# Optimization experiments

Hardware: AMD Instinct MI355X
Metric: run time of the kernel (lower is better)

The kernel has to match this reference:

```python
import jax, jax.numpy as jnp
import numpy as np

B, V, H = 128, 50257, 2048   # batch, vocab, history length
NEG_INF = jnp.float32(-jnp.inf)
TEMP_MIN = 1e-5


def setup_inputs() -> dict:
    key = jax.random.key(0)
    k1, k2, k3 = jax.random.split(key, 3)
    logits = jax.random.normal(k1, (B, V), jnp.float32) * 4.0
    previous_tokens = jax.random.randint(k2, (B, H), 0, V)
    # uniform noise for the exponential-race (Gumbel-max) draw; strictly positive
    u = jax.random.uniform(k3, (B, V), jnp.float32, minval=1e-10, maxval=1.0)
    return {
        "logits": logits,
        "previous_tokens": previous_tokens,
        "u": u,
        "top_p": jnp.full((1,), 0.9, jnp.float32),
        "repetition_penalty": jnp.full((1,), 1.35, jnp.float32),
        "temperature": jnp.full((1,), 0.7, jnp.float32),
        "top_k": 50,
    }


def _logits_to_probs(logits, previous_tokens, temperature, top_k, top_p, repetition_penalty):
    b = jnp.arange(logits.shape[0])[:, None]  # [B,1] row index for scatters
    # repetition penalty: gather history scores, shrink, scatter back
    score = jnp.take_along_axis(logits, previous_tokens, axis=1)          # [B,H]
    score = jnp.where(score < 0, score * repetition_penalty, score / repetition_penalty)
    logits = logits.at[b, previous_tokens].set(score)                     # [B,V]
    # nucleus (top-p) filtering via descending sort + cumulative softmax
    order = jnp.argsort(-logits, axis=-1)                                 # [B,V]
    sorted_logits = jnp.take_along_axis(logits, order, axis=1)
    cum_probs = jnp.cumsum(jax.nn.softmax(sorted_logits, axis=-1), axis=-1)
    remove_sorted = cum_probs > top_p
    remove_sorted = remove_sorted.at[:, 0].set(False)                     # keep best token
    # scatter removal mask back to vocab order (order is a permutation)
    remove = jnp.zeros_like(remove_sorted).at[b, order].set(remove_sorted)
    logits = jnp.where(remove, NEG_INF, logits)
    # temperature + top-k pivot filter
    logits = logits / jnp.maximum(temperature, TEMP_MIN)
    v = jax.lax.top_k(logits, top_k)[0]                                   # [B,top_k]
    pivot = v[:, -1:]
    logits = jnp.where(logits < pivot, NEG_INF, logits)
    return jax.nn.softmax(logits, axis=-1)


def reference(logits, previous_tokens, u, top_p, repetition_penalty, temperature, top_k):
    previous_tokens = previous_tokens.astype(jnp.int32)
    probs = _logits_to_probs(logits, previous_tokens, temperature, top_k, top_p,
                             repetition_penalty)
    # multinomial_sample_one_no_sync: exponential race argmax(probs / Exp(1))
    q = -jnp.log(u)
    idx_next = jnp.argmax(probs / q, axis=-1, keepdims=True).astype(jnp.int32)
    return idx_next, probs
```

## Files before the change

kernel.cpp:

```cpp
#include <hip/hip_runtime.h>
#include <cfloat>
#include <cmath>
#include <cstdint>

#define VV 50257
#define SPLITS 8
#define CHUNKA 6284
#define BMW ((CHUNKA + 31) / 32)
#define CAPC 256
#define K1T 256
#define NWAVE (K1T / 64)
#define K2T 512
#define CEXP 28.0f

__device__ __forceinline__ unsigned fmono(float f) {
    unsigned b = __float_as_uint(f);
    return b ^ (((int)b < 0) ? 0xFFFFFFFFu : 0x80000000u);
}
__device__ __forceinline__ float unmono(unsigned m) {
    unsigned b = (m & 0x80000000u) ? (m ^ 0x80000000u) : ~m;
    return __uint_as_float(b);
}
__device__ __forceinline__ uint64_t mkkey(unsigned mono, int idx) {
    return ((uint64_t)mono << 32) | (unsigned)(~idx);
}

__global__ __launch_bounds__(K1T) void pp_k1(
    const float* __restrict__ logits, const int* __restrict__ prev,
    const float* __restrict__ rpp,
    float* __restrict__ ps, uint64_t* __restrict__ gkey,
    float* __restrict__ out_probs, int Hp)
{
    const int sp = blockIdx.x, row = blockIdx.y;
    const int tid = threadIdx.x, lane = tid & 63, wid = tid >> 6;
    const int c0 = sp * CHUNKA;
    const int c1 = min(VV, c0 + CHUNKA);
    const int len = c1 - c0;
    const float rp = rpp[0], inv_rp = 1.0f / rp;

    __shared__ unsigned bm[BMW];
    __shared__ float vals[CHUNKA];
    __shared__ uint64_t kls[K1T];
    __shared__ uint64_t cand[CAPC];
    __shared__ uint64_t top64[64];
    __shared__ float red_s[NWAVE];
    __shared__ uint64_t sV64;
    __shared__ int sCnt, sCnt2;

    for (int i = tid; i < BMW; i += K1T) bm[i] = 0u;
    if (tid == 0) sCnt = 0;
    __syncthreads();

    const int* prow = prev + (size_t)row * Hp;
    const int h4 = Hp >> 2;
    const int4* prow4 = (const int4*)prow;
    for (int i = tid; i < h4; i += K1T) {
        int4 t4 = prow4[i];
        int t;
        t = t4.x; if (t >= c0 && t < c1) { int o = t - c0; atomicOr(&bm[o >> 5], 1u << (o & 31)); }
        t = t4.y; if (t >= c0 && t < c1) { int o = t - c0; atomicOr(&bm[o >> 5], 1u << (o & 31)); }
        t = t4.z; if (t >= c0 && t < c1) { int o = t - c0; atomicOr(&bm[o >> 5], 1u << (o & 31)); }
        t = t4.w; if (t >= c0 && t < c1) { int o = t - c0; atomicOr(&bm[o >> 5], 1u << (o & 31)); }
    }
    for (int i = 4 * h4 + tid; i < Hp; i += K1T) {
        int t = prow[i];
        if (t >= c0 && t < c1) { int o = t - c0; atomicOr(&bm[o >> 5], 1u << (o & 31)); }
    }
    __syncthreads();

    const float* lrow = logits + (size_t)row * VV;
    float* orow = out_probs + (size_t)row * VV;
    const int pad = (4 - (row & 3)) & 3;
    const int n4 = (len - pad) >> 2;
    const int tail0 = pad + 4 * n4;
    const float4* l4 = (const float4*)(lrow + c0 + pad);
    float4* o4 = (float4*)(orow + c0 + pad);
    const float4 z4 = make_float4(0.f, 0.f, 0.f, 0.f);

    float s = 0.0f;
    uint64_t k0 = 0ull;
    for (int o = tid; o < pad; o += K1T) {
        float x = lrow[c0 + o];
        if ((bm[o >> 5] >> (o & 31)) & 1u) x = (x < 0.f) ? x * rp : x * inv_rp;
        vals[o] = x;
        s += __expf(x - CEXP);
        uint64_t a = mkkey(fmono(x), c0 + o);
        k0 = (a > k0) ? a : k0;
    }
    #pragma unroll 4
    for (int k = tid; k < n4; k += K1T) {
        float4 v = l4[k];
        const int ob = pad + 4 * k;
        float x;
        x = v.x; if ((bm[(ob+0) >> 5] >> ((ob+0) & 31)) & 1u) x = (x < 0.f) ? x * rp : x * inv_rp;
        vals[ob + 0] = x; s += __expf(x - CEXP);
        { uint64_t a = mkkey(fmono(x), c0 + ob + 0); k0 = (a > k0) ? a : k0; }
        x = v.y; if ((bm[(ob+1) >> 5] >> ((ob+1) & 31)) & 1u) x = (x < 0.f) ? x * rp : x * inv_rp;
        vals[ob + 1] = x; s += __expf(x - CEXP);
        { uint64_t a = mkkey(fmono(x), c0 + ob + 1); k0 = (a > k0) ? a : k0; }
        x = v.z; if ((bm[(ob+2) >> 5] >> ((ob+2) & 31)) & 1u) x = (x < 0.f) ? x * rp : x * inv_rp;
        vals[ob + 2] = x; s += __expf(x - CEXP);
        { uint64_t a = mkkey(fmono(x), c0 + ob + 2); k0 = (a > k0) ? a : k0; }
        x = v.w; if ((bm[(ob+3) >> 5] >> ((ob+3) & 31)) & 1u) x = (x < 0.f) ? x * rp : x * inv_rp;
        vals[ob + 3] = x; s += __expf(x - CEXP);
        { uint64_t a = mkkey(fmono(x), c0 + ob + 3); k0 = (a > k0) ? a : k0; }
    }
    for (int o = tail0 + tid; o < len; o += K1T) {
        float x = lrow[c0 + o];
        if ((bm[o >> 5] >> (o & 31)) & 1u) x = (x < 0.f) ? x * rp : x * inv_rp;
        vals[o] = x;
        s += __expf(x - CEXP);
        uint64_t a = mkkey(fmono(x), c0 + o);
        k0 = (a > k0) ? a : k0;
    }

    #pragma unroll
    for (int off = 32; off; off >>= 1) s += __shfl_down(s, off);
    if (lane == 0) red_s[wid] = s;

    {
        uint64_t v = k0;
        #pragma unroll
        for (int kk = 2; kk <= 64; kk <<= 1) {
            #pragma unroll
            for (int j = kk >> 1; j > 0; j >>= 1) {
                uint64_t o = __shfl_xor(v, j);
                bool lower = (lane & j) == 0;
                bool asc = (lane & kk) == 0;
                uint64_t mx = (v > o) ? v : o;
                uint64_t mn = (v > o) ? o : v;
                v = (lower != asc) ? mx : mn;
            }
        }
        kls[wid * 64 + (63 - lane)] = v;
    }
    __syncthreads();

    const int slot = row * SPLITS + sp;
    if (tid == 0) {
        float S = red_s[0];
        #pragma unroll
        for (int w = 1; w < NWAVE; ++w) S += red_s[w];
        ps[slot] = S;
    }

    {
        const uint64_t ki = kls[tid];
        int r = tid & 63;
        const int j = tid >> 6;
        #pragma unroll
        for (int o = 0; o < NWAVE; ++o) {
            if (o == j) continue;
            const uint64_t* ls = &kls[o * 64];
            int lo = 0, hi = 64;
            while (lo < hi) {
                int mid = (lo + hi) >> 1;
                if (ls[mid] > ki) lo = mid + 1; else hi = mid;
            }
            r += lo;
        }
        if (r == 63) sV64 = ki;
    }
    __syncthreads();
    const uint64_t th = sV64;

    for (int o = tid; o < len; o += K1T) {
        float x = vals[o];
        uint64_t a = mkkey(fmono(x), c0 + o);
        if (a >= th) {
            int p = atomicAdd(&sCnt, 1);
            if (p < CAPC) cand[p] = a;
        }
    }
    __syncthreads();
    int cnt = sCnt;

    for (int o = tid; o < pad; o += K1T) orow[c0 + o] = 0.0f;
    for (int k = tid; k < n4; k += K1T) o4[k] = z4;
    for (int o = tail0 + tid; o < len; o += K1T) orow[c0 + o] = 0.0f;

    if (cnt > CAPC) {
        uint64_t loK = th, hiK = ~0ull;
        uint64_t thF = th;
        for (int it = 0; it < 64; ++it) {
            uint64_t mid = loK + ((hiK - loK) >> 1);
            if (mid == loK) { thF = hiK; break; }
            if (tid == 0) sCnt2 = 0;
            __syncthreads();
            int lc = 0;
            for (int o = tid; o < len; o += K1T) {
                float x = vals[o];
                lc += (int)(mkkey(fmono(x), c0 + o) >= mid);
            }
            #pragma unroll
            for (int off = 32; off; off >>= 1) lc += __shfl_down(lc, off);
            if (lane == 0) atomicAdd(&sCnt2, lc);
            __syncthreads();
            int c = sCnt2;
            __syncthreads();
            if (c >= 64 && c <= CAPC) { thF = mid; break; }
            if (c > CAPC) loK = mid; else hiK = mid;
        }
        if (tid == 0) sCnt = 0;
        __syncthreads();
        for (int o = tid; o < len; o += K1T) {
            float x = vals[o];
            uint64_t a = mkkey(fmono(x), c0 + o);
            if (a >= thF) {
                int p = atomicAdd(&sCnt, 1);
                if (p < CAPC) cand[p] = a;
            }
        }
        __syncthreads();
        cnt = min(sCnt, CAPC);
    }

    for (int t = tid; t < cnt; t += K1T) {
        const uint64_t ki = cand[t];
        int r = 0;
        int j = 0;
        for (; j + 8 <= cnt; j += 8) {
            uint64_t a0 = cand[j],   a1 = cand[j+1], a2 = cand[j+2], a3 = cand[j+3];
            uint64_t a4 = cand[j+4], a5 = cand[j+5], a6 = cand[j+6], a7 = cand[j+7];
            r += (int)(a0 > ki) + (int)(a1 > ki) + (int)(a2 > ki) + (int)(a3 > ki)
               + (int)(a4 > ki) + (int)(a5 > ki) + (int)(a6 > ki) + (int)(a7 > ki);
        }
        for (; j < cnt; ++j) r += (int)(cand[j] > ki);
        if (r < 64) top64[r] = ki;
    }
    __syncthreads();
    if (tid < 64) gkey[(size_t)slot * 64 + tid] = top64[tid];
}

__global__ __launch_bounds__(K2T) void pp_k2(
    const float* __restrict__ u, const float* __restrict__ toppp,
    const float* __restrict__ tempp, const int* __restrict__ topkp,
    const float* __restrict__ ps, const uint64_t* __restrict__ gkey,
    float* __restrict__ out_idx, float* __restrict__ out_probs)
{
    const int row = blockIdx.x, tid = threadIdx.x;
    __shared__ uint64_t ck[SPLITS * 64];
    __shared__ uint64_t tk[64];
    __shared__ float sS;

    ck[tid] = gkey[(size_t)row * (SPLITS * 64) + tid];
    if (tid == 0) {
        float S = 0.0f;
        #pragma unroll
        for (int j = 0; j < SPLITS; ++j) S += ps[row * SPLITS + j];
        sS = S;
    }
    __syncthreads();

    {
        const int j = tid >> 6;
        const uint64_t ki = ck[tid];
        int r = tid & 63;
        #pragma unroll
        for (int o = 0; o < SPLITS; ++o) {
            if (o == j) continue;
            const uint64_t* ls = &ck[o * 64];
            int lo = 0, hi = 64;
            while (lo < hi) {
                int mid = (lo + hi) >> 1;
                if (ls[mid] > ki) lo = mid + 1; else hi = mid;
            }
            r += lo;
        }
        if (r < 64) tk[r] = ki;
    }
    __syncthreads();

    if (tid < 64) {
        const int lane = tid;
        const float top_p = toppp[0];
        const float temp = tempp[0];
        int K = topkp[0]; K = min(max(K, 1), 64);
        const float Ssum = sS;
        const uint64_t k64 = tk[lane];
        const float vl = unmono((unsigned)(k64 >> 32));
        const int ci = (int)(~(unsigned)(k64 & 0xFFFFFFFFu));
        bool act = (lane < K);
        float e = act ? expf(vl - CEXP) / Ssum : 0.0f;
        float cum = e;
        #pragma unroll
        for (int off2 = 1; off2 < 64; off2 <<= 1) {
            float pv = __shfl_up(cum, off2);
            if (lane >= off2) cum += pv;
        }
        unsigned long long bal = __ballot(act && (cum <= top_p));
        int n = (int)__popcll(bal);
        if (n < 1) n = 1;
        const float v0 = __shfl(vl, 0);
        const float invT = 1.0f / fmaxf(temp, 1e-5f);
        bool keep = (lane < n);
        float w = keep ? expf((vl - v0) * invT) : 0.0f;
        float Z = w;
        #pragma unroll
        for (int off2 = 32; off2; off2 >>= 1) Z += __shfl_xor(Z, off2);
        float p = keep ? (w / Z) : 0.0f;
        if (keep) out_probs[(size_t)row * VV + ci] = p;
        float ratio = -1.0f;
        if (keep) ratio = p / (-logf(u[(size_t)row * VV + ci]));
        int bi = keep ? ci : 0x7FFFFFFF;
        #pragma unroll
        for (int off2 = 32; off2; off2 >>= 1) {
            float orat = __shfl_xor(ratio, off2);
            int oidx = __shfl_xor(bi, off2);
            if (orat > ratio || (orat == ratio && oidx < bi)) { ratio = orat; bi = oidx; }
        }
        if (lane == 0) out_idx[row] = (float)bi;
    }
}

extern "C" void kernel_launch(void* const* d_in, const int* in_sizes, int n_in,
                              void* d_out, int out_size, void* d_ws, size_t ws_size,
                              hipStream_t stream) {
    const float* logits = (const float*)d_in[0];
    const int*   prev   = (const int*)d_in[1];
    const float* u      = (const float*)d_in[2];
    const float* topp   = (const float*)d_in[3];
    const float* rp     = (const float*)d_in[4];
    const float* temp   = (const float*)d_in[5];
    const int*   topk   = (const int*)d_in[6];

    const int B  = in_sizes[0] / VV;
    const int Hp = in_sizes[1] / B;

    char* ws = (char*)d_ws;
    float* ps = (float*)ws;
    uint64_t* gkey = (uint64_t*)(ws + 16384);

    float* out = (float*)d_out;
    pp_k1<<<dim3(SPLITS, B), K1T, 0, stream>>>(
        logits, prev, rp, ps, gkey, out + B, Hp);
    pp_k2<<<B, K2T, 0, stream>>>(
        u, topp, temp, topk, ps, gkey, out, out + B);
}
```

Measured before the change: 31.89 us.

## Drop LDS value staging, re-read logits from global, double block size

Removes the 25KB shared-memory array holding penalized chunk values. The candidate pass and fallback search now reload logits from global memory (likely L2-resident) and reapply the penalty. The output-zeroing stores are folded into the first load loop, and threads per block and candidate capacity are doubled to 512. The intent is higher occupancy with less LDS and more parallel threads per chunk, at the cost of a second global read of each chunk and recomputing the penalty.

```diff
diff --git a/kernel.cpp b/kernel.cpp
--- a/kernel.cpp
+++ b/kernel.cpp
@@ -7,8 +7,8 @@
 #define SPLITS 8
 #define CHUNKA 6284
 #define BMW ((CHUNKA + 31) / 32)
-#define CAPC 256
-#define K1T 256
+#define CAPC 512
+#define K1T 512
 #define NWAVE (K1T / 64)
 #define K2T 512
 #define CEXP 28.0f
@@ -39,7 +39,6 @@
     const float rp = rpp[0], inv_rp = 1.0f / rp;
 
     __shared__ unsigned bm[BMW];
-    __shared__ float vals[CHUNKA];
     __shared__ uint64_t kls[K1T];
     __shared__ uint64_t cand[CAPC];
     __shared__ uint64_t top64[64];
@@ -77,12 +76,18 @@
     float4* o4 = (float4*)(orow + c0 + pad);
     const float4 z4 = make_float4(0.f, 0.f, 0.f, 0.f);
 
+    auto keyAt = [&](int o) -> uint64_t {
+        float x = lrow[c0 + o];
+        if ((bm[o >> 5] >> (o & 31)) & 1u) x = (x < 0.f) ? x * rp : x * inv_rp;
+        return mkkey(fmono(x), c0 + o);
+    };
+
     float s = 0.0f;
     uint64_t k0 = 0ull;
     for (int o = tid; o < pad; o += K1T) {
         float x = lrow[c0 + o];
+        orow[c0 + o] = 0.0f;
         if ((bm[o >> 5] >> (o & 31)) & 1u) x = (x < 0.f) ? x * rp : x * inv_rp;
-        vals[o] = x;
         s += __expf(x - CEXP);
         uint64_t a = mkkey(fmono(x), c0 + o);
         k0 = (a > k0) ? a : k0;
@@ -90,25 +95,26 @@
     #pragma unroll 4
     for (int k = tid; k < n4; k += K1T) {
         float4 v = l4[k];
+        o4[k] = z4;
         const int ob = pad + 4 * k;
         float x;
         x = v.x; if ((bm[(ob+0) >> 5] >> ((ob+0) & 31)) & 1u) x = (x < 0.f) ? x * rp : x * inv_rp;
-        vals[ob + 0] = x; s += __expf(x - CEXP);
+        s += __expf(x - CEXP);
         { uint64_t a = mkkey(fmono(x), c0 + ob + 0); k0 = (a > k0) ? a : k0; }
         x = v.y; if ((bm[(ob+1) >> 5] >> ((ob+1) & 31)) & 1u) x = (x < 0.f) ? x * rp : x * inv_rp;
-        vals[ob + 1] = x; s += __expf(x - CEXP);
+        s += __expf(x - CEXP);
         { uint64_t a = mkkey(fmono(x), c0 + ob + 1); k0 = (a > k0) ? a : k0; }
         x = v.z; if ((bm[(ob+2) >> 5] >> ((ob+2) & 31)) & 1u) x = (x < 0.f) ? x * rp : x * inv_rp;
-        vals[ob + 2] = x; s += __expf(x - CEXP);
+        s += __expf(x - CEXP);
         { uint64_t a = mkkey(fmono(x), c0 + ob + 2); k0 = (a > k0) ? a : k0; }
         x = v.w; if ((bm[(ob+3) >> 5] >> ((ob+3) & 31)) & 1u) x = (x < 0.f) ? x * rp : x * inv_rp;
-        vals[ob + 3] = x; s += __expf(x - CEXP);
+        s += __expf(x - CEXP);
         { uint64_t a = mkkey(fmono(x), c0 + ob + 3); k0 = (a > k0) ? a : k0; }
     }
     for (int o = tail0 + tid; o < len; o += K1T) {
         float x = lrow[c0 + o];
+        orow[c0 + o] = 0.0f;
         if ((bm[o >> 5] >> (o & 31)) & 1u) x = (x < 0.f) ? x * rp : x * inv_rp;
-        vals[o] = x;
         s += __expf(x - CEXP);
         uint64_t a = mkkey(fmono(x), c0 + o);
         k0 = (a > k0) ? a : k0;
@@ -164,34 +170,40 @@
     __syncthreads();
     const uint64_t th = sV64;
 
-    for (int o = tid; o < len; o += K1T) {
-        float x = vals[o];
-        uint64_t a = mkkey(fmono(x), c0 + o);
-        if (a >= th) {
-            int p = atomicAdd(&sCnt, 1);
-            if (p < CAPC) cand[p] = a;
-        }
+    for (int o = tid; o < pad; o += K1T) {
+        uint64_t a = keyAt(o);
+        if (a >= th) { int p = atomicAdd(&sCnt, 1); if (p < CAPC) cand[p] = a; }
+    }
+    #pragma unroll 2
+    for (int k = tid; k < n4; k += K1T) {
+        float4 v = l4[k];
+        const int ob = pad + 4 * k;
+        float x;
+        x = v.x; if ((bm[(ob+0) >> 5] >> ((ob+0) & 31)) & 1u) x = (x < 0.f) ? x * rp : x * inv_rp;
+        { uint64_t a = mkkey(fmono(x), c0 + ob + 0); if (a >= th) { int p = atomicAdd(&sCnt, 1); if (p < CAPC) cand[p] = a; } }
+        x = v.y; if ((bm[(ob+1) >> 5] >> ((ob+1) & 31)) & 1u) x = (x < 0.f) ? x * rp : x * inv_rp;
+        { uint64_t a = mkkey(fmono(x), c0 + ob + 1); if (a >= th) { int p = atomicAdd(&sCnt, 1); if (p < CAPC) cand[p] = a; } }
+        x = v.z; if ((bm[(ob+2) >> 5] >> ((ob+2) & 31)) & 1u) x = (x < 0.f) ? x * rp : x * inv_rp;
+        { uint64_t a = mkkey(fmono(x), c0 + ob + 2); if (a >= th) { int p = atomicAdd(&sCnt, 1); if (p < CAPC) cand[p] = a; } }
+        x = v.w; if ((bm[(ob+3) >> 5] >> ((ob+3) & 31)) & 1u) x = (x < 0.f) ? x * rp : x * inv_rp;
+        { uint64_t a = mkkey(fmono(x), c0 + ob + 3); if (a >= th) { int p = atomicAdd(&sCnt, 1); if (p < CAPC) cand[p] = a; } }
+    }
+    for (int o = tail0 + tid; o < len; o += K1T) {
+        uint64_t a = keyAt(o);
+        if (a >= th) { int p = atomicAdd(&sCnt, 1); if (p < CAPC) cand[p] = a; }
     }
     __syncthreads();
     int cnt = sCnt;
 
-    for (int o = tid; o < pad; o += K1T) orow[c0 + o] = 0.0f;
-    for (int k = tid; k < n4; k += K1T) o4[k] = z4;
-    for (int o = tail0 + tid; o < len; o += K1T) orow[c0 + o] = 0.0f;
-
     if (cnt > CAPC) {
-        uint64_t loK = th, hiK = ~0ull;
-        uint64_t thF = th;
+        uint64_t loK = th, hiK = ~0ull, thF = th;
         for (int it = 0; it < 64; ++it) {
             uint64_t mid = loK + ((hiK - loK) >> 1);
             if (mid == loK) { thF = hiK; break; }
             if (tid == 0) sCnt2 = 0;
             __syncthreads();
             int lc = 0;
-            for (int o = tid; o < len; o += K1T) {
-                float x = vals[o];
-                lc += (int)(mkkey(fmono(x), c0 + o) >= mid);
-            }
+            for (int o = tid; o < len; o += K1T) lc += (int)(keyAt(o) >= mid);
             #pragma unroll
             for (int off = 32; off; off >>= 1) lc += __shfl_down(lc, off);
             if (lane == 0) atomicAdd(&sCnt2, lc);
@@ -204,12 +216,8 @@
         if (tid == 0) sCnt = 0;
         __syncthreads();
         for (int o = tid; o < len; o += K1T) {
-            float x = vals[o];
-            uint64_t a = mkkey(fmono(x), c0 + o);
-            if (a >= thF) {
-                int p = atomicAdd(&sCnt, 1);
-                if (p < CAPC) cand[p] = a;
-            }
+            uint64_t a = keyAt(o);
+            if (a >= thF) { int p = atomicAdd(&sCnt, 1); if (p < CAPC) cand[p] = a; }
         }
         __syncthreads();
         cnt = min(sCnt, CAPC);
```

New measurement: 35.92 us. 12.6% more time.
